# Kernel tuning notes

Measured on AMD Instinct MI355X. Metric: run time of the kernel, lower is better.

## Reference

```python
import jax, jax.numpy as jnp
import numpy as np

DN = ('NCHW', 'OIHW', 'NCHW')

def conv3x3(x, w, b):
    y = jax.lax.conv_general_dilated(x, w, window_strides=(1, 1), padding='SAME', dimension_numbers=DN)
    return y + b[None, :, None, None]

def setup_inputs() -> dict:
    key = jax.random.key(0)
    ks = jax.random.split(key, 7)
    B, Cin, C, H, W = 16, 256, 256, 128, 128
    fan_in = Cin * 9
    s = 1.0 / np.sqrt(fan_in)
    x = jax.random.normal(ks[0], (B, Cin, H, W), dtype=jnp.float32)
    Wq = jax.random.uniform(ks[1], (C, Cin, 3, 3), jnp.float32, -s, s)
    bq = jax.random.uniform(ks[2], (C,), jnp.float32, -s, s)
    Wk = jax.random.uniform(ks[3], (C, Cin, 3, 3), jnp.float32, -s, s)
    bk = jax.random.uniform(ks[4], (C,), jnp.float32, -s, s)
    Wv = jax.random.uniform(ks[5], (C, Cin, 3, 3), jnp.float32, -s, s)
    bv = jax.random.uniform(ks[6], (C,), jnp.float32, -s, s)
    return {"x": x, "Wq": Wq, "bq": bq, "Wk": Wk, "bk": bk, "Wv": Wv, "bv": bv}

def reference(x, Wq, bq, Wk, bk, Wv, bv):
    # QKV via 3x3 convs: [B,C,H,W]
    q = conv3x3(x, Wq, bq)
    k = conv3x3(x, Wk, bk)
    v = conv3x3(x, Wv, bv)
    d_k = q.shape[-1]  # W (last dim), matching torch query.size(-1)
    # scores: per (B,C), [H,H] = q[H,W] @ k[H,W]^T
    scores = jnp.einsum('bchw,bcgw->bchg', q, k) / jnp.sqrt(jnp.asarray(d_k, q.dtype))
    p = jax.nn.softmax(scores, axis=-1)  # [B,C,H,H]
    out = jnp.einsum('bchg,bcgw->bchw', p, v)  # [B,C,H,W]
    return out
```

## Files before the change

kernel.cpp:

```cpp
#include <hip/hip_runtime.h>
#include <stdint.h>

typedef __attribute__((ext_vector_type(8))) short bf16x8;
typedef __attribute__((ext_vector_type(4))) float f32x4;
typedef __attribute__((ext_vector_type(8))) unsigned short us8;

__device__ __forceinline__ unsigned short f2bf(float f) {
  unsigned u = __builtin_bit_cast(unsigned, f);
  return (unsigned short)((u + 0x7FFFu + ((u >> 16) & 1u)) >> 16);
}

#define GLD16(g, l)                                                            \
  __builtin_amdgcn_global_load_lds(                                            \
      (const __attribute__((address_space(1))) unsigned int*)(g),              \
      (__attribute__((address_space(3))) unsigned int*)(l), 16, 0, 0)

__global__ void prep_w(const float* __restrict__ wq, const float* __restrict__ wk,
                       const float* __restrict__ wv, unsigned short* __restrict__ wt) {
  int idx = blockIdx.x * 256 + threadIdx.x;
  int ci = idx & 255;
  int t = idx >> 8;
  int cg = t % 768;
  int khw = t / 768;
  int kh = khw / 3, kw = khw % 3;
  int conv = cg >> 8, cl = cg & 255;
  const float* src = conv == 0 ? wq : (conv == 1 ? wk : wv);
  wt[idx] = f2bf(src[((cl * 256 + ci) * 3 + kh) * 3 + kw]);
}

__global__ void prep_x(const float* __restrict__ x, unsigned short* __restrict__ xt) {
  __shared__ unsigned short xs[64][130];
  const int tid = threadIdx.x;
  const int ci0 = blockIdx.x * 64;
  const int h = blockIdx.y;
  const int b = blockIdx.z;
#pragma unroll
  for (int i = 0; i < 8; ++i) {
    int f = tid + 256 * i;
    int r = f >> 5, w4 = f & 31;
    f32x4 v = *(const f32x4*)(x + (((size_t)(b * 256 + ci0 + r) * 128 + h) * 128 + w4 * 4));
    xs[r][w4 * 4 + 0] = f2bf(v[0]);
    xs[r][w4 * 4 + 1] = f2bf(v[1]);
    xs[r][w4 * 4 + 2] = f2bf(v[2]);
    xs[r][w4 * 4 + 3] = f2bf(v[3]);
  }
  __syncthreads();
#pragma unroll
  for (int i = 0; i < 4; ++i) {
    int q = tid + 256 * i;
    int w = q >> 3, jc = q & 7;
    us8 o;
#pragma unroll
    for (int j = 0; j < 8; ++j) o[j] = xs[jc * 8 + j][w];
    *(us8*)(xt + ((size_t)(b * 128 + h) * 128 + w) * 256 + ci0 + jc * 8) = o;
  }
}

__global__ __launch_bounds__(256, 2) void conv_qkv(
    const unsigned short* __restrict__ xt, const unsigned short* __restrict__ wt,
    const float* __restrict__ bq, const float* __restrict__ bk,
    const float* __restrict__ bv, unsigned short* __restrict__ qkout,
    unsigned short* __restrict__ vout) {
  __shared__ unsigned short As[3 * 8192];
  __shared__ unsigned short Xs[8192];
  const int tid = threadIdx.x;
  const int lane = tid & 63;
  const int wid = tid >> 6;
  const int wm = wid >> 1, wn = wid & 1;
  const int l15 = lane & 15, l4 = lane >> 4;
  const int ct = blockIdx.x;
  const int h = blockIdx.y;
  const int b = blockIdx.z;
  const int cg0 = ct * 128;

  f32x4 acc[4][4] = {};

  for (int kh = 0; kh < 3; ++kh) {
    const int hs = h + kh - 1;
    if (hs < 0 || hs > 127) continue;
    const unsigned short* xrow = xt + (size_t)(b * 128 + hs) * 128 * 256;
    const unsigned short* wbase = wt + (size_t)(kh * 3) * 768 * 256;
    for (int ch = 0; ch < 4; ++ch) {
      const int ci0 = ch * 64;
      __syncthreads();
#pragma unroll
      for (int ii = 0; ii < 4; ++ii) {
        int i = wid * 4 + ii;
        int cidx = i * 64 + lane;
        int w = cidx >> 3, j = cidx & 7;
        int jg = j ^ (w & 7);
        GLD16(xrow + w * 256 + ci0 + jg * 8, (char*)Xs + i * 1024);
      }
#pragma unroll
      for (int ii = 0; ii < 12; ++ii) {
        int i = wid * 12 + ii;
        int cidx = i * 64 + lane;
        int kw = cidx >> 10, cc = cidx & 1023;
        int row = cc >> 3, j = cc & 7;
        int jg = j ^ (row & 7);
        GLD16(wbase + (size_t)(kw * 768 + cg0 + row) * 256 + ci0 + jg * 8,
              (char*)As + i * 1024);
      }
      __syncthreads();
#pragma unroll
      for (int kw = 0; kw < 3; ++kw) {
#pragma unroll
        for (int kp = 0; kp < 2; ++kp) {
          const int ko = (kp * 32 + l4 * 8) * 2;
          bf16x8 a[4], bb[4];
#pragma unroll
          for (int mf = 0; mf < 4; ++mf) {
            int row = wm * 64 + mf * 16 + l15;
            a[mf] = *(const bf16x8*)((const char*)As + kw * 16384 + row * 128 +
                                     (ko ^ ((row & 7) << 4)));
          }
#pragma unroll
          for (int nf = 0; nf < 4; ++nf) {
            int w = wn * 64 + nf * 16 + l15;
            int rr = w + kw - 1;
            int rc = rr < 0 ? 0 : (rr > 127 ? 127 : rr);
            bf16x8 t = *(const bf16x8*)((const char*)Xs + rc * 128 +
                                        (ko ^ ((rc & 7) << 4)));
            if (rr != rc) t = bf16x8{0, 0, 0, 0, 0, 0, 0, 0};
            bb[nf] = t;
          }
#pragma unroll
          for (int mf = 0; mf < 4; ++mf)
#pragma unroll
            for (int nf = 0; nf < 4; ++nf)
              acc[mf][nf] = __builtin_amdgcn_mfma_f32_16x16x32_bf16(
                  a[mf], bb[nf], acc[mf][nf], 0, 0, 0);
        }
      }
    }
  }

  const int conv = ct >> 1;
  const float* bias = conv == 0 ? bq : (conv == 1 ? bk : bv);
  unsigned short* outp = conv == 0 ? qkout : (conv == 1 ? qkout + 16384 : vout);
  const int per_bc = conv == 2 ? 16384 : 32768;
#pragma unroll
  for (int mf = 0; mf < 4; ++mf)
#pragma unroll
    for (int r = 0; r < 4; ++r) {
      int crow = (ct & 1) * 128 + wm * 64 + mf * 16 + l4 * 4 + r;
      float bia = bias[crow];
      unsigned short* dst = outp + (size_t)(b * 256 + crow) * per_bc + h * 128;
#pragma unroll
      for (int nf = 0; nf < 4; ++nf) {
        int w = wn * 64 + nf * 16 + l15;
        dst[w] = f2bf(acc[mf][nf][r] + bia);
      }
    }
}

__global__ __launch_bounds__(256, 2) void attn_kernel(
    const unsigned short* qkbuf, const unsigned short* __restrict__ vbuf,
    float* out) {
  __shared__ unsigned short qs[16384];
  __shared__ unsigned short ks[16384];
  const int tid = threadIdx.x;
  const int lane = tid & 63;
  const int wid = tid >> 6;
  const int l15 = lane & 15, l4 = lane >> 4;
  const int bc = blockIdx.y * 256 + blockIdx.x;

  const unsigned short* vsrc = vbuf + (size_t)bc * 16384;
  const int vs = tid & 15;
  const int vg0 = (tid >> 4) * 8;
  uint4 vreg[8];
#pragma unroll
  for (int i = 0; i < 8; ++i)
    vreg[i] = *(const uint4*)(vsrc + (vg0 + i) * 128 + vs * 8);

  const unsigned short* qsrc = qkbuf + (size_t)bc * 32768;
  const unsigned short* ksrc = qsrc + 16384;
#pragma unroll
  for (int ii = 0; ii < 8; ++ii) {
    int i = wid * 8 + ii;
    int t2 = i * 64 + lane;
    int row = t2 >> 4, s = t2 & 15;
    int sg = s ^ (row & 7);
    GLD16(qsrc + row * 128 + sg * 8, (char*)qs + i * 1024);
    GLD16(ksrc + row * 128 + sg * 8, (char*)ks + i * 1024);
  }
  __syncthreads();

  f32x4 acc[2][8] = {};
#pragma unroll
  for (int kp = 0; kp < 4; ++kp) {
    int ko = (kp * 32 + l4 * 8) * 2;
    bf16x8 a[2], bb[8];
#pragma unroll
    for (int mf = 0; mf < 2; ++mf) {
      int hh = wid * 32 + mf * 16 + l15;
      a[mf] = *(const bf16x8*)((const char*)qs + hh * 256 + (ko ^ ((hh & 7) << 4)));
    }
#pragma unroll
    for (int nf = 0; nf < 8; ++nf) {
      int g = nf * 16 + l15;
      bb[nf] = *(const bf16x8*)((const char*)ks + g * 256 + (ko ^ ((g & 7) << 4)));
    }
#pragma unroll
    for (int mf = 0; mf < 2; ++mf)
#pragma unroll
      for (int nf = 0; nf < 8; ++nf)
        acc[mf][nf] =
            __builtin_amdgcn_mfma_f32_16x16x32_bf16(a[mf], bb[nf], acc[mf][nf], 0, 0, 0);
  }
  __syncthreads();

#pragma unroll
  for (int j = 0; j < 8; ++j) {
    int w = vs * 8 + j;
    us8 o;
#pragma unroll
    for (int i = 0; i < 8; ++i) o[i] = ((const unsigned short*)&vreg[i])[j];
    int chunk = (vg0 >> 3) ^ (w & 7) ^ ((w >> 3) & 7);
    *(us8*)((char*)ks + w * 256 + (chunk << 4)) = o;
  }

  const float SC = 0.088388347648318447f;
#pragma unroll
  for (int mf = 0; mf < 2; ++mf)
#pragma unroll
    for (int nf = 0; nf < 8; ++nf) acc[mf][nf] *= SC;
#pragma unroll
  for (int mf = 0; mf < 2; ++mf) {
#pragma unroll
    for (int r = 0; r < 4; ++r) {
      float m = acc[mf][0][r];
#pragma unroll
      for (int nf = 1; nf < 8; ++nf) m = fmaxf(m, acc[mf][nf][r]);
      m = fmaxf(m, __shfl_xor(m, 1));
      m = fmaxf(m, __shfl_xor(m, 2));
      m = fmaxf(m, __shfl_xor(m, 4));
      m = fmaxf(m, __shfl_xor(m, 8));
      float p[8], ssum = 0.f;
#pragma unroll
      for (int nf = 0; nf < 8; ++nf) {
        p[nf] = __expf(acc[mf][nf][r] - m);
        ssum += p[nf];
      }
      ssum += __shfl_xor(ssum, 1);
      ssum += __shfl_xor(ssum, 2);
      ssum += __shfl_xor(ssum, 4);
      ssum += __shfl_xor(ssum, 8);
      float inv = 1.f / ssum;
      int hh = wid * 32 + mf * 16 + l4 * 4 + r;
      int swz = (hh & 7) << 4;
#pragma unroll
      for (int nf = 0; nf < 8; ++nf) {
        int g = nf * 16 + l15;
        *(unsigned short*)((char*)qs + hh * 256 + ((2 * g) ^ swz)) = f2bf(p[nf] * inv);
      }
    }
  }
  __syncthreads();

  f32x4 o[2][8] = {};
#pragma unroll
  for (int kp = 0; kp < 4; ++kp) {
    int ko = (kp * 32 + l4 * 8) * 2;
    bf16x8 pa[2], vb[8];
#pragma unroll
    for (int mf = 0; mf < 2; ++mf) {
      int hh = wid * 32 + mf * 16 + l15;
      pa[mf] = *(const bf16x8*)((const char*)qs + hh * 256 + (ko ^ ((hh & 7) << 4)));
    }
#pragma unroll
    for (int nf = 0; nf < 8; ++nf) {
      int w = nf * 16 + l15;
      int chunk = (ko >> 4) ^ (w & 7) ^ ((w >> 3) & 7);
      vb[nf] = *(const bf16x8*)((const char*)ks + w * 256 + (chunk << 4));
    }
#pragma unroll
    for (int mf = 0; mf < 2; ++mf)
#pragma unroll
      for (int nf = 0; nf < 8; ++nf)
        o[mf][nf] =
            __builtin_amdgcn_mfma_f32_16x16x32_bf16(pa[mf], vb[nf], o[mf][nf], 0, 0, 0);
  }
  float* ob = out + (size_t)bc * 16384;
#pragma unroll
  for (int mf = 0; mf < 2; ++mf)
#pragma unroll
    for (int r = 0; r < 4; ++r) {
      int hh = wid * 32 + mf * 16 + l4 * 4 + r;
#pragma unroll
      for (int nf = 0; nf < 8; ++nf) {
        int w = nf * 16 + l15;
        ob[hh * 128 + w] = o[mf][nf][r];
      }
    }
}

extern "C" void kernel_launch(void* const* d_in, const int* in_sizes, int n_in,
                              void* d_out, int out_size, void* d_ws, size_t ws_size,
                              hipStream_t stream) {
  const float* x = (const float*)d_in[0];
  const float* wq = (const float*)d_in[1];
  const float* bq = (const float*)d_in[2];
  const float* wk = (const float*)d_in[3];
  const float* bk = (const float*)d_in[4];
  const float* wv = (const float*)d_in[5];
  const float* bv = (const float*)d_in[6];

  char* ws = (char*)d_ws;
  unsigned short* xt = (unsigned short*)ws;
  unsigned short* wt = (unsigned short*)(ws + 134217728);
  unsigned short* vbuf = (unsigned short*)(ws + 134217728 + 3538944);

  prep_w<<<6912, 256, 0, stream>>>(wq, wk, wv, wt);
  prep_x<<<dim3(4, 128, 16), 256, 0, stream>>>(x, xt);
  conv_qkv<<<dim3(6, 128, 16), 256, 0, stream>>>(
      xt, wt, bq, bk, bv, (unsigned short*)d_out, vbuf);
  attn_kernel<<<dim3(256, 16), 256, 0, stream>>>(
      (const unsigned short*)d_out, vbuf, (float*)d_out);
}
```

Before: 1.367 ms.

## Double-buffer conv weight tiles, enlarge M tile, remap blocks for XCD locality

The conv kernel now computes a 256-channel tile per block (acc[8][4]) instead of 128, so each staged input row is reused across twice as many output channels. Weight tiles are split per kw into two LDS slots and loaded with explicit vmcnt waits and raw barriers, so the next kw's load overlaps the current MFMA work, with raised priority during compute. The 1D grid is remapped so consecutive blocks on the same XCD share h/b rows, to improve L2 reuse. prep_x drops its LDS transpose in favour of a register transpose. The larger accumulator raises register pressure and may reduce occupancy.

```diff
diff --git a/kernel.cpp b/kernel.cpp
--- a/kernel.cpp
+++ b/kernel.cpp
@@ -14,6 +14,19 @@
   __builtin_amdgcn_global_load_lds(                                            \
       (const __attribute__((address_space(1))) unsigned int*)(g),              \
       (__attribute__((address_space(3))) unsigned int*)(l), 16, 0, 0)
+
+#define SCHED0() __builtin_amdgcn_sched_barrier(0)
+#define SBAR()                                                                 \
+  do {                                                                         \
+    SCHED0();                                                                  \
+    __builtin_amdgcn_s_barrier();                                              \
+    SCHED0();                                                                  \
+  } while (0)
+#define WAITVM(n)                                                              \
+  do {                                                                         \
+    asm volatile("s_waitcnt vmcnt(" #n ")" ::: "memory");                      \
+    SCHED0();                                                                  \
+  } while (0)
 
 __global__ void prep_w(const float* __restrict__ wq, const float* __restrict__ wk,
                        const float* __restrict__ wv, unsigned short* __restrict__ wt) {
@@ -29,30 +42,23 @@
 }
 
 __global__ void prep_x(const float* __restrict__ x, unsigned short* __restrict__ xt) {
-  __shared__ unsigned short xs[64][130];
   const int tid = threadIdx.x;
+  const int jc = tid >> 5, wg = tid & 31;
   const int ci0 = blockIdx.x * 64;
   const int h = blockIdx.y;
   const int b = blockIdx.z;
-#pragma unroll
-  for (int i = 0; i < 8; ++i) {
-    int f = tid + 256 * i;
-    int r = f >> 5, w4 = f & 31;
-    f32x4 v = *(const f32x4*)(x + (((size_t)(b * 256 + ci0 + r) * 128 + h) * 128 + w4 * 4));
-    xs[r][w4 * 4 + 0] = f2bf(v[0]);
-    xs[r][w4 * 4 + 1] = f2bf(v[1]);
-    xs[r][w4 * 4 + 2] = f2bf(v[2]);
-    xs[r][w4 * 4 + 3] = f2bf(v[3]);
-  }
-  __syncthreads();
-#pragma unroll
-  for (int i = 0; i < 4; ++i) {
-    int q = tid + 256 * i;
-    int w = q >> 3, jc = q & 7;
+  f32x4 v[8];
+#pragma unroll
+  for (int j = 0; j < 8; ++j)
+    v[j] = *(const f32x4*)(x + (((size_t)(b * 256 + ci0 + jc * 8 + j)) * 128 + h) * 128 +
+                           wg * 4);
+  unsigned short* dst = xt + ((size_t)(b * 128 + h) * 128) * 256 + ci0 + jc * 8;
+#pragma unroll
+  for (int m = 0; m < 4; ++m) {
     us8 o;
 #pragma unroll
-    for (int j = 0; j < 8; ++j) o[j] = xs[jc * 8 + j][w];
-    *(us8*)(xt + ((size_t)(b * 128 + h) * 128 + w) * 256 + ci0 + jc * 8) = o;
+    for (int j = 0; j < 8; ++j) o[j] = f2bf(v[j][m]);
+    *(us8*)(dst + (wg * 4 + m) * 256) = o;
   }
 }
 
@@ -61,89 +67,104 @@
     const float* __restrict__ bq, const float* __restrict__ bk,
     const float* __restrict__ bv, unsigned short* __restrict__ qkout,
     unsigned short* __restrict__ vout) {
-  __shared__ unsigned short As[3 * 8192];
   __shared__ unsigned short Xs[8192];
+  __shared__ unsigned short As[2][16384];
   const int tid = threadIdx.x;
   const int lane = tid & 63;
   const int wid = tid >> 6;
   const int wm = wid >> 1, wn = wid & 1;
   const int l15 = lane & 15, l4 = lane >> 4;
-  const int ct = blockIdx.x;
-  const int h = blockIdx.y;
-  const int b = blockIdx.z;
-  const int cg0 = ct * 128;
-
-  f32x4 acc[4][4] = {};
+  const int n = blockIdx.x;
+  const int lg = (n & 7) * 768 + (n >> 3);
+  const int ct = lg % 3;
+  const int rest = lg / 3;
+  const int h = rest & 127, b = rest >> 7;
+  const int cg0 = ct * 256;
+
+  f32x4 acc[8][4] = {};
+
+  auto stageX = [&](const unsigned short* xsrc) {
+#pragma unroll
+    for (int ii = 0; ii < 4; ++ii) {
+      int i = wid * 4 + ii;
+      int cidx = i * 64 + lane;
+      int w = cidx >> 3, j = cidx & 7;
+      GLD16(xsrc + w * 256 + (j ^ (w & 7)) * 8, (char*)Xs + i * 1024);
+    }
+  };
+  auto stageA = [&](const unsigned short* asrc, unsigned short* slot) {
+#pragma unroll
+    for (int ii = 0; ii < 8; ++ii) {
+      int i = wid * 8 + ii;
+      int cidx = i * 64 + lane;
+      int row = cidx >> 3, j = cidx & 7;
+      GLD16(asrc + row * 256 + (j ^ (row & 7)) * 8, (char*)slot + i * 1024);
+    }
+  };
+  auto compute = [&](const unsigned short* slot, int kw) {
+    __builtin_amdgcn_s_setprio(1);
+#pragma unroll
+    for (int kp = 0; kp < 2; ++kp) {
+      const int ko = (kp * 32 + l4 * 8) * 2;
+      bf16x8 bfr[4];
+#pragma unroll
+      for (int nf = 0; nf < 4; ++nf) {
+        int w = wn * 64 + nf * 16 + l15;
+        int rr = w + kw - 1;
+        int rc = rr < 0 ? 0 : (rr > 127 ? 127 : rr);
+        bf16x8 t =
+            *(const bf16x8*)((const char*)Xs + rc * 128 + (ko ^ ((rc & 7) << 4)));
+        if (rr != rc) t = (bf16x8){0, 0, 0, 0, 0, 0, 0, 0};
+        bfr[nf] = t;
+      }
+#pragma unroll
+      for (int mf = 0; mf < 8; ++mf) {
+        int row = wm * 128 + mf * 16 + l15;
+        bf16x8 af =
+            *(const bf16x8*)((const char*)slot + row * 128 + (ko ^ ((row & 7) << 4)));
+#pragma unroll
+        for (int nf = 0; nf < 4; ++nf)
+          acc[mf][nf] = __builtin_amdgcn_mfma_f32_16x16x32_bf16(af, bfr[nf],
+                                                               acc[mf][nf], 0, 0, 0);
+      }
+    }
+    __builtin_amdgcn_s_setprio(0);
+  };
 
   for (int kh = 0; kh < 3; ++kh) {
     const int hs = h + kh - 1;
     if (hs < 0 || hs > 127) continue;
-    const unsigned short* xrow = xt + (size_t)(b * 128 + hs) * 128 * 256;
-    const unsigned short* wbase = wt + (size_t)(kh * 3) * 768 * 256;
+    const unsigned short* xrow = xt + (size_t)(b * 128 + hs) * 32768;
+    const unsigned short* wk0 = wt + ((size_t)(kh * 3) * 768 + cg0) * 256;
+#pragma unroll 1
     for (int ch = 0; ch < 4; ++ch) {
       const int ci0 = ch * 64;
-      __syncthreads();
-#pragma unroll
-      for (int ii = 0; ii < 4; ++ii) {
-        int i = wid * 4 + ii;
-        int cidx = i * 64 + lane;
-        int w = cidx >> 3, j = cidx & 7;
-        int jg = j ^ (w & 7);
-        GLD16(xrow + w * 256 + ci0 + jg * 8, (char*)Xs + i * 1024);
-      }
-#pragma unroll
-      for (int ii = 0; ii < 12; ++ii) {
-        int i = wid * 12 + ii;
-        int cidx = i * 64 + lane;
-        int kw = cidx >> 10, cc = cidx & 1023;
-        int row = cc >> 3, j = cc & 7;
-        int jg = j ^ (row & 7);
-        GLD16(wbase + (size_t)(kw * 768 + cg0 + row) * 256 + ci0 + jg * 8,
-              (char*)As + i * 1024);
-      }
-      __syncthreads();
-#pragma unroll
-      for (int kw = 0; kw < 3; ++kw) {
-#pragma unroll
-        for (int kp = 0; kp < 2; ++kp) {
-          const int ko = (kp * 32 + l4 * 8) * 2;
-          bf16x8 a[4], bb[4];
-#pragma unroll
-          for (int mf = 0; mf < 4; ++mf) {
-            int row = wm * 64 + mf * 16 + l15;
-            a[mf] = *(const bf16x8*)((const char*)As + kw * 16384 + row * 128 +
-                                     (ko ^ ((row & 7) << 4)));
-          }
-#pragma unroll
-          for (int nf = 0; nf < 4; ++nf) {
-            int w = wn * 64 + nf * 16 + l15;
-            int rr = w + kw - 1;
-            int rc = rr < 0 ? 0 : (rr > 127 ? 127 : rr);
-            bf16x8 t = *(const bf16x8*)((const char*)Xs + rc * 128 +
-                                        (ko ^ ((rc & 7) << 4)));
-            if (rr != rc) t = bf16x8{0, 0, 0, 0, 0, 0, 0, 0};
-            bb[nf] = t;
-          }
-#pragma unroll
-          for (int mf = 0; mf < 4; ++mf)
-#pragma unroll
-            for (int nf = 0; nf < 4; ++nf)
-              acc[mf][nf] = __builtin_amdgcn_mfma_f32_16x16x32_bf16(
-                  a[mf], bb[nf], acc[mf][nf], 0, 0, 0);
-        }
-      }
-    }
-  }
-
-  const int conv = ct >> 1;
-  const float* bias = conv == 0 ? bq : (conv == 1 ? bk : bv);
-  unsigned short* outp = conv == 0 ? qkout : (conv == 1 ? qkout + 16384 : vout);
-  const int per_bc = conv == 2 ? 16384 : 32768;
-#pragma unroll
-  for (int mf = 0; mf < 4; ++mf)
+      SBAR();
+      stageX(xrow + ci0);
+      stageA(wk0 + ci0, As[0]);
+      stageA(wk0 + 196608 + ci0, As[1]);
+      WAITVM(8);
+      SBAR();
+      compute(As[0], 0);
+      SBAR();
+      stageA(wk0 + 393216 + ci0, As[0]);
+      WAITVM(8);
+      SBAR();
+      compute(As[1], 1);
+      WAITVM(0);
+      SBAR();
+      compute(As[0], 2);
+    }
+  }
+
+  const float* bias = ct == 0 ? bq : (ct == 1 ? bk : bv);
+  unsigned short* outp = ct == 0 ? qkout : (ct == 1 ? qkout + 16384 : vout);
+  const int per_bc = ct == 2 ? 16384 : 32768;
+#pragma unroll
+  for (int mf = 0; mf < 8; ++mf)
 #pragma unroll
     for (int r = 0; r < 4; ++r) {
-      int crow = (ct & 1) * 128 + wm * 64 + mf * 16 + l4 * 4 + r;
+      int crow = wm * 128 + mf * 16 + l4 * 4 + r;
       float bia = bias[crow];
       unsigned short* dst = outp + (size_t)(b * 256 + crow) * per_bc + h * 128;
 #pragma unroll
@@ -313,8 +334,8 @@
 
   prep_w<<<6912, 256, 0, stream>>>(wq, wk, wv, wt);
   prep_x<<<dim3(4, 128, 16), 256, 0, stream>>>(x, xt);
-  conv_qkv<<<dim3(6, 128, 16), 256, 0, stream>>>(
-      xt, wt, bq, bk, bv, (unsigned short*)d_out, vbuf);
-  attn_kernel<<<dim3(256, 16), 256, 0, stream>>>(
-      (const unsigned short*)d_out, vbuf, (float*)d_out);
-}
+  conv_qkv<<<6144, 256, 0, stream>>>(xt, wt, bq, bk, bv, (unsigned short*)d_out,
+                                     vbuf);
+  attn_kernel<<<dim3(256, 16), 256, 0, stream>>>((const unsigned short*)d_out, vbuf,
+                                                 (float*)d_out);
+}
```

After: 1.276 ms. -6.6%, faster.
